# Kernel optimization log

Hardware: AMD Instinct MI355X
Metric: run time of the kernel (lower is better)

## Reference

```python
import jax, jax.numpy as jnp
import numpy as np

B, S, D = 4, 2048, 1024
H, Dh = 16, 64


def setup_inputs() -> dict:
    key = jax.random.key(0)
    ks = jax.random.split(key, 9)
    s_in = 1.0 / np.sqrt(D)
    inp = {
        "key": jax.random.normal(ks[0], (B, S, D), jnp.float32),
        "value": jax.random.normal(ks[1], (B, S, D), jnp.float32),
        "query": jax.random.normal(ks[2], (B, S, D), jnp.float32),
        # Linear weights stored as [in, out] (math-equivalent to torch W.T)
        "Wq": jax.random.uniform(ks[3], (D, H * Dh), jnp.float32, -s_in, s_in),
        "bq": jax.random.uniform(ks[4], (H * Dh,), jnp.float32, -s_in, s_in),
        "Wk": jax.random.uniform(ks[5], (D, H * Dh), jnp.float32, -s_in, s_in),
        "bk": jax.random.uniform(ks[6], (H * Dh,), jnp.float32, -s_in, s_in),
        "Wv": jax.random.uniform(ks[7], (D, H * Dh), jnp.float32, -s_in, s_in),
        "bv": jax.random.uniform(ks[8], (H * Dh,), jnp.float32, -s_in, s_in),
    }
    return inp


def reference(key, value, query, Wq, bq, Wk, bk, Wv, bv):
    b, s, _ = key.shape
    # projections -> [B, H, S, Dh]
    q = (query @ Wq + bq).reshape(b, s, H, Dh).transpose(0, 2, 1, 3)
    k = (key @ Wk + bk).reshape(b, s, H, Dh).transpose(0, 2, 1, 3)
    v = (value @ Wv + bv).reshape(b, s, H, Dh).transpose(0, 2, 1, 3)
    scores = jnp.einsum("bhqd,bhkd->bhqk", q, k) / np.sqrt(Dh).astype(np.float32)
    p = jax.nn.softmax(scores, axis=-1)
    out = jnp.einsum("bhqk,bhkd->bhqd", p, v)  # [B, H, S, Dh]
    return out.transpose(0, 2, 1, 3).reshape(b, s, H * Dh)
```

## Files before the change

kernel.cpp:

```cpp
#include <hip/hip_runtime.h>

typedef __bf16 bf16;
typedef __bf16 bf16x8 __attribute__((ext_vector_type(8)));
typedef __bf16 bf16x4 __attribute__((ext_vector_type(4)));
typedef _Float16 f16x4 __attribute__((ext_vector_type(4)));
typedef float  f32x4  __attribute__((ext_vector_type(4)));

#define LOG2E 1.44269504088896340736f
#define SCQ (0.125f * LOG2E)

__device__ __forceinline__ void async16(const void* g, void* l) {
  __builtin_amdgcn_global_load_lds(
      (const __attribute__((address_space(1))) unsigned int*)g,
      (__attribute__((address_space(3))) unsigned int*)l, 16, 0, 0);
}

__device__ __forceinline__ f32x4 mfma_bf16(bf16x8 a, bf16x8 b, f32x4 c) {
  return __builtin_amdgcn_mfma_f32_16x16x32_bf16(a, b, c, 0, 0, 0);
}
__device__ __forceinline__ f32x4 mfma_f16k16(f16x4 a, f16x4 b, f32x4 c) {
  return __builtin_amdgcn_mfma_f32_16x16x16f16(a, b, c, 0, 0, 0);
}

__global__ __launch_bounds__(256) void cvt3(const float* __restrict__ q,
                                            const float* __restrict__ k,
                                            const float* __restrict__ v,
                                            bf16* __restrict__ out) {
  int z = blockIdx.y;
  const float* in = z == 0 ? q : (z == 1 ? k : v);
  bf16* o = out + (size_t)z * 8388608;
  int i = blockIdx.x * 256 + threadIdx.x;
  const float4* p = (const float4*)in;
  float4 a = p[i * 2], c = p[i * 2 + 1];
  bf16x8 r;
  r[0] = (bf16)a.x; r[1] = (bf16)a.y; r[2] = (bf16)a.z; r[3] = (bf16)a.w;
  r[4] = (bf16)c.x; r[5] = (bf16)c.y; r[6] = (bf16)c.z; r[7] = (bf16)c.w;
  ((bf16x8*)o)[i] = r;
}

__global__ __launch_bounds__(256) void wtrans(const float* __restrict__ W0,
                                              const float* __restrict__ W1,
                                              const float* __restrict__ W2,
                                              bf16* __restrict__ Wt) {
  const float* W = blockIdx.z == 0 ? W0 : (blockIdx.z == 1 ? W1 : W2);
  bf16* O = Wt + (size_t)blockIdx.z * (1024 * 1024);
  __shared__ float t[64 * 69];
  int tid = threadIdx.x;
  int k0 = blockIdx.x * 64, n0 = blockIdx.y * 64;
  int r0 = tid >> 4, c0 = (tid & 15) * 4;
#pragma unroll
  for (int rr = 0; rr < 4; rr++) {
    int k = r0 + rr * 16;
    float4 v = *(const float4*)(W + (k0 + k) * 1024 + n0 + c0);
    t[k * 69 + c0 + 0] = v.x; t[k * 69 + c0 + 1] = v.y;
    t[k * 69 + c0 + 2] = v.z; t[k * 69 + c0 + 3] = v.w;
  }
  __syncthreads();
#pragma unroll
  for (int rr = 0; rr < 4; rr++) {
    int n = r0 + rr * 16;
    bf16x4 o;
#pragma unroll
    for (int j = 0; j < 4; j++) o[j] = (bf16)t[(c0 + j) * 69 + n];
    *(bf16x4*)(O + (n0 + n) * 1024 + k0 + c0) = o;
  }
}

__global__ __launch_bounds__(256) void gemm_qkv(const bf16* __restrict__ Act,
                                                const bf16* __restrict__ Wt,
                                                const float* __restrict__ b0,
                                                const float* __restrict__ b1,
                                                const float* __restrict__ b2,
                                                bf16* __restrict__ qo,
                                                bf16* __restrict__ ko,
                                                _Float16* __restrict__ vf) {
  __shared__ bf16 smem[16384];
  bf16* sA = smem;
  bf16* sB = smem + 8192;
  const int tid = threadIdx.x;
  const int wave = tid >> 6, lane = tid & 63;
  const int quad = lane >> 4, l15 = lane & 15;
  const int z = blockIdx.z;
  const int m0 = blockIdx.x * 128, n0 = blockIdx.y * 128;
  const bf16* A = Act + (size_t)z * 8388608;
  const bf16* Bt = Wt + (size_t)z * 1048576;
  const float* bias = z == 0 ? b0 : (z == 1 ? b1 : b2);

  const bf16* ap[4]; const bf16* bp[4]; int lo[4];
#pragma unroll
  for (int i = 0; i < 4; i++) {
    int g = wave * 256 + i * 64 + lane;
    int row = g >> 3, jl = (g & 7) ^ (row & 7);
    ap[i] = A + (m0 + row) * 1024 + jl * 8;
    bp[i] = Bt + (n0 + row) * 1024 + jl * 8;
    lo[i] = (wave * 256 + i * 64) * 8;
  }
  const int wm = (wave & 1) * 64, wn = (wave >> 1) * 64;
  f32x4 acc[4][4] = {};

  for (int kt = 0; kt < 16; kt++) {
    const int ko_ = kt * 64;
#pragma unroll
    for (int i = 0; i < 4; i++) async16(ap[i] + ko_, sA + lo[i]);
#pragma unroll
    for (int i = 0; i < 4; i++) async16(bp[i] + ko_, sB + lo[i]);
    __syncthreads();
#pragma unroll
    for (int ks = 0; ks < 2; ks++) {
      bf16x8 af[4], bv[4];
#pragma unroll
      for (int mt = 0; mt < 4; mt++) {
        int m = wm + mt * 16 + l15;
        int ph = (ks * 4 + quad) ^ (m & 7);
        af[mt] = *(const bf16x8*)(sA + m * 64 + ph * 8);
      }
#pragma unroll
      for (int nt = 0; nt < 4; nt++) {
        int n = wn + nt * 16 + l15;
        int ph = (ks * 4 + quad) ^ (n & 7);
        bv[nt] = *(const bf16x8*)(sB + n * 64 + ph * 8);
      }
#pragma unroll
      for (int mt = 0; mt < 4; mt++)
#pragma unroll
        for (int nt = 0; nt < 4; nt++)
          acc[mt][nt] = mfma_bf16(af[mt], bv[nt], acc[mt][nt]);
    }
    __syncthreads();
  }

  if (z != 2) {
    bf16* O = z == 0 ? qo : ko;
    const float sc = z == 0 ? SCQ : 1.0f;
#pragma unroll
    for (int nt = 0; nt < 4; nt++) {
      int n = n0 + wn + nt * 16 + l15;
      float bc = bias[n];
#pragma unroll
      for (int mt = 0; mt < 4; mt++)
#pragma unroll
        for (int r = 0; r < 4; r++) {
          int m = m0 + wm + mt * 16 + quad * 4 + r;
          O[m * 1024 + n] = (bf16)((acc[mt][nt][r] + bc) * sc);
        }
    }
  } else {
    const int b = m0 >> 11, s0 = m0 & 2047;
    const int kvb = (s0 + wm) >> 6;
#pragma unroll
    for (int nt = 0; nt < 4; nt++) {
      int nn = n0 + wn + nt * 16;
      int h = nn >> 6, dt = (nn >> 4) & 3;
      float bc = bias[nn + l15];
#pragma unroll
      for (int mt = 0; mt < 4; mt++) {
        f16x4 pk;
#pragma unroll
        for (int r = 0; r < 4; r++) pk[r] = (_Float16)(acc[mt][nt][r] + bc);
        size_t off = ((((size_t)(b * 16 + h) * 32 + kvb) * 16 + (mt * 4 + dt)) * 64 + lane) * 4;
        *(f16x4*)(vf + off) = pk;
      }
    }
  }
}

__global__ __launch_bounds__(256) void attn(const bf16* __restrict__ Q,
                                            const bf16* __restrict__ K,
                                            const _Float16* __restrict__ VF,
                                            float* __restrict__ Out) {
  __shared__ bf16 sQ[8192];
  __shared__ bf16 sK[2][4096];
  __shared__ _Float16 sV[2][4096];
  const int tid = threadIdx.x;
  const int wave = tid >> 6, lane = tid & 63;
  const int quad = lane >> 4, l15 = lane & 15;
  const int q0 = blockIdx.x * 128, h = blockIdx.y, b = blockIdx.z;
  const bf16* Kbase = K + (size_t)(b * 2048) * 1024 + h * 64;
  const _Float16* Vbase = VF + (size_t)(b * 16 + h) * 131072;

#pragma unroll
  for (int i = 0; i < 4; i++) {
    int g = i * 256 + tid;
    int row = g >> 3, jl = (g & 7) ^ (row & 7);
    async16(Q + (size_t)(b * 2048 + q0 + row) * 1024 + h * 64 + jl * 8, sQ + g * 8);
  }
#pragma unroll
  for (int i = 0; i < 2; i++) {
    int g = i * 256 + tid;
    int row = g >> 3, jl = (g & 7) ^ (row & 7);
    async16(Kbase + row * 1024 + jl * 8, sK[0] + g * 8);
    async16(Vbase + g * 8, sV[0] + g * 8);
  }
  __syncthreads();

  bf16x8 qf[2][2];
#pragma unroll
  for (int qt2 = 0; qt2 < 2; qt2++)
#pragma unroll
    for (int ks = 0; ks < 2; ks++) {
      int m = wave * 32 + qt2 * 16 + l15;
      int ph = (ks * 4 + quad) ^ (l15 & 7);
      qf[qt2][ks] = *(const bf16x8*)(sQ + m * 64 + ph * 8);
    }

  f32x4 oaccT[2][4] = {};
  float ls[2] = {0.f, 0.f};

  const int ph0 = quad ^ (l15 & 7), ph1 = (4 + quad) ^ (l15 & 7);

  for (int kvb = 0; kvb < 32; kvb++) {
    const int cur = kvb & 1;
    if (kvb < 31) {
      int kn = (kvb + 1) * 64;
#pragma unroll
      for (int i = 0; i < 2; i++) {
        int g = i * 256 + tid;
        int row = g >> 3, jl = (g & 7) ^ (row & 7);
        async16(Kbase + (size_t)(kn + row) * 1024 + jl * 8, sK[cur ^ 1] + g * 8);
        async16(Vbase + (kvb + 1) * 4096 + g * 8, sV[cur ^ 1] + g * 8);
      }
    }
    const bf16* sKc = sK[cur];
    const _Float16* sVc = sV[cur];
#pragma unroll
    for (int t = 0; t < 4; t++) {
      int row = t * 16 + l15;
      bf16x8 kf0 = *(const bf16x8*)(sKc + row * 64 + ph0 * 8);
      bf16x8 kf1 = *(const bf16x8*)(sKc + row * 64 + ph1 * 8);
      f32x4 st0 = {}, st1 = {};
      st0 = mfma_bf16(kf0, qf[0][0], st0);
      st0 = mfma_bf16(kf1, qf[0][1], st0);
      st1 = mfma_bf16(kf0, qf[1][0], st1);
      st1 = mfma_bf16(kf1, qf[1][1], st1);
      f16x4 pf0, pf1;
#pragma unroll
      for (int r = 0; r < 4; r++) {
        float p0 = __builtin_amdgcn_exp2f(st0[r]);
        float p1 = __builtin_amdgcn_exp2f(st1[r]);
        ls[0] += p0; ls[1] += p1;
        pf0[r] = (_Float16)p0; pf1[r] = (_Float16)p1;
      }
#pragma unroll
      for (int dt = 0; dt < 4; dt++) {
        f16x4 va = *(const f16x4*)(sVc + ((t * 4 + dt) * 64 + lane) * 4);
        oaccT[0][dt] = mfma_f16k16(va, pf0, oaccT[0][dt]);
        oaccT[1][dt] = mfma_f16k16(va, pf1, oaccT[1][dt]);
      }
    }
    __syncthreads();
  }

#pragma unroll
  for (int qt2 = 0; qt2 < 2; qt2++) {
    float l = ls[qt2];
    l += __shfl_xor(l, 16);
    l += __shfl_xor(l, 32);
    float inv = 1.f / l;
    int qrow = b * 2048 + q0 + wave * 32 + qt2 * 16 + l15;
#pragma unroll
    for (int dt = 0; dt < 4; dt++) {
      float4 v;
      v.x = oaccT[qt2][dt][0] * inv;
      v.y = oaccT[qt2][dt][1] * inv;
      v.z = oaccT[qt2][dt][2] * inv;
      v.w = oaccT[qt2][dt][3] * inv;
      *(float4*)(Out + (size_t)qrow * 1024 + h * 64 + dt * 16 + quad * 4) = v;
    }
  }
}

extern "C" void kernel_launch(void* const* d_in, const int* in_sizes, int n_in,
                              void* d_out, int out_size, void* d_ws, size_t ws_size,
                              hipStream_t stream) {
  const float* key   = (const float*)d_in[0];
  const float* value = (const float*)d_in[1];
  const float* query = (const float*)d_in[2];
  const float* Wq = (const float*)d_in[3];
  const float* bq = (const float*)d_in[4];
  const float* Wk = (const float*)d_in[5];
  const float* bk = (const float*)d_in[6];
  const float* Wv = (const float*)d_in[7];
  const float* bv = (const float*)d_in[8];
  float* out = (float*)d_out;

  char* ws = (char*)d_ws;
  bf16* actb   = (bf16*)(ws);
  bf16* wt     = (bf16*)(ws + 50331648);
  bf16* qo     = (bf16*)(ws + 56623104);
  bf16* ko     = (bf16*)(ws + 73400320);
  _Float16* vf = (_Float16*)(ws + 90177536);
  (void)in_sizes; (void)n_in; (void)out_size; (void)ws_size;

  wtrans<<<dim3(16, 16, 3), 256, 0, stream>>>(Wq, Wk, Wv, wt);
  cvt3<<<dim3(4096, 3), 256, 0, stream>>>(query, key, value, actb);
  gemm_qkv<<<dim3(64, 8, 3), 256, 0, stream>>>(actb, wt, bq, bk, bv, qo, ko, vf);
  attn<<<dim3(16, 16, 4), 256, 0, stream>>>(qo, ko, vf, out);
}
```

Measured before the change: 335.6 us.

## Enlarge GEMM tile to 128x256 with swizzled grid; single-buffer 128-key attention tiles

The QKV GEMM now computes 128x256 tiles per block, with each wave holding a 64x128 accumulator. Block indices are remapped through a swizzle for L2 locality, the launch gets min-blocks hints, and the grid is halved. The attention kernel drops K/V double-buffering in favour of single 128-key tiles loaded synchronously after each tile is consumed, with an occupancy hint of 4 blocks. This cuts per-tile overhead and barrier count, but loses load/compute overlap within a block and raises register pressure.

```diff
diff --git a/kernel.cpp b/kernel.cpp
--- a/kernel.cpp
+++ b/kernel.cpp
@@ -66,48 +66,58 @@
   }
 }
 
-__global__ __launch_bounds__(256) void gemm_qkv(const bf16* __restrict__ Act,
-                                                const bf16* __restrict__ Wt,
-                                                const float* __restrict__ b0,
-                                                const float* __restrict__ b1,
-                                                const float* __restrict__ b2,
-                                                bf16* __restrict__ qo,
-                                                bf16* __restrict__ ko,
-                                                _Float16* __restrict__ vf) {
-  __shared__ bf16 smem[16384];
+__global__ __launch_bounds__(256, 2) void gemm_qkv(const bf16* __restrict__ Act,
+                                                   const bf16* __restrict__ Wt,
+                                                   const float* __restrict__ b0,
+                                                   const float* __restrict__ b1,
+                                                   const float* __restrict__ b2,
+                                                   bf16* __restrict__ qo,
+                                                   bf16* __restrict__ ko,
+                                                   _Float16* __restrict__ vf) {
+  __shared__ bf16 smem[24576];
   bf16* sA = smem;
   bf16* sB = smem + 8192;
   const int tid = threadIdx.x;
   const int wave = tid >> 6, lane = tid & 63;
   const int quad = lane >> 4, l15 = lane & 15;
   const int z = blockIdx.z;
-  const int m0 = blockIdx.x * 128, n0 = blockIdx.y * 128;
+  const int lin = blockIdx.y * 64 + blockIdx.x;
+  const int tx = (lin & 7) | ((lin >> 5) << 3);
+  const int ty = (lin >> 3) & 3;
+  const int m0 = tx * 128, n0 = ty * 256;
   const bf16* A = Act + (size_t)z * 8388608;
   const bf16* Bt = Wt + (size_t)z * 1048576;
   const float* bias = z == 0 ? b0 : (z == 1 ? b1 : b2);
 
-  const bf16* ap[4]; const bf16* bp[4]; int lo[4];
+  const bf16* ap[4]; int loa[4];
+  const bf16* bp[8]; int lob[8];
 #pragma unroll
   for (int i = 0; i < 4; i++) {
     int g = wave * 256 + i * 64 + lane;
     int row = g >> 3, jl = (g & 7) ^ (row & 7);
     ap[i] = A + (m0 + row) * 1024 + jl * 8;
+    loa[i] = (wave * 256 + i * 64) * 8;
+  }
+#pragma unroll
+  for (int i = 0; i < 8; i++) {
+    int g = wave * 512 + i * 64 + lane;
+    int row = g >> 3, jl = (g & 7) ^ (row & 7);
     bp[i] = Bt + (n0 + row) * 1024 + jl * 8;
-    lo[i] = (wave * 256 + i * 64) * 8;
-  }
-  const int wm = (wave & 1) * 64, wn = (wave >> 1) * 64;
-  f32x4 acc[4][4] = {};
+    lob[i] = (wave * 512 + i * 64) * 8;
+  }
+  const int wm = (wave & 1) * 64, wn = (wave >> 1) * 128;
+  f32x4 acc[4][8] = {};
 
   for (int kt = 0; kt < 16; kt++) {
     const int ko_ = kt * 64;
 #pragma unroll
-    for (int i = 0; i < 4; i++) async16(ap[i] + ko_, sA + lo[i]);
-#pragma unroll
-    for (int i = 0; i < 4; i++) async16(bp[i] + ko_, sB + lo[i]);
+    for (int i = 0; i < 4; i++) async16(ap[i] + ko_, sA + loa[i]);
+#pragma unroll
+    for (int i = 0; i < 8; i++) async16(bp[i] + ko_, sB + lob[i]);
     __syncthreads();
 #pragma unroll
     for (int ks = 0; ks < 2; ks++) {
-      bf16x8 af[4], bv[4];
+      bf16x8 af[4];
 #pragma unroll
       for (int mt = 0; mt < 4; mt++) {
         int m = wm + mt * 16 + l15;
@@ -115,16 +125,20 @@
         af[mt] = *(const bf16x8*)(sA + m * 64 + ph * 8);
       }
 #pragma unroll
-      for (int nt = 0; nt < 4; nt++) {
-        int n = wn + nt * 16 + l15;
-        int ph = (ks * 4 + quad) ^ (n & 7);
-        bv[nt] = *(const bf16x8*)(sB + n * 64 + ph * 8);
-      }
-#pragma unroll
-      for (int mt = 0; mt < 4; mt++)
-#pragma unroll
-        for (int nt = 0; nt < 4; nt++)
-          acc[mt][nt] = mfma_bf16(af[mt], bv[nt], acc[mt][nt]);
+      for (int nh = 0; nh < 2; nh++) {
+        bf16x8 bv[4];
+#pragma unroll
+        for (int nt = 0; nt < 4; nt++) {
+          int n = wn + (nh * 4 + nt) * 16 + l15;
+          int ph = (ks * 4 + quad) ^ (n & 7);
+          bv[nt] = *(const bf16x8*)(sB + n * 64 + ph * 8);
+        }
+#pragma unroll
+        for (int mt = 0; mt < 4; mt++)
+#pragma unroll
+          for (int nt = 0; nt < 4; nt++)
+            acc[mt][nh * 4 + nt] = mfma_bf16(af[mt], bv[nt], acc[mt][nh * 4 + nt]);
+      }
     }
     __syncthreads();
   }
@@ -133,7 +147,7 @@
     bf16* O = z == 0 ? qo : ko;
     const float sc = z == 0 ? SCQ : 1.0f;
 #pragma unroll
-    for (int nt = 0; nt < 4; nt++) {
+    for (int nt = 0; nt < 8; nt++) {
       int n = n0 + wn + nt * 16 + l15;
       float bc = bias[n];
 #pragma unroll
@@ -148,7 +162,7 @@
     const int b = m0 >> 11, s0 = m0 & 2047;
     const int kvb = (s0 + wm) >> 6;
 #pragma unroll
-    for (int nt = 0; nt < 4; nt++) {
+    for (int nt = 0; nt < 8; nt++) {
       int nn = n0 + wn + nt * 16;
       int h = nn >> 6, dt = (nn >> 4) & 3;
       float bc = bias[nn + l15];
@@ -164,13 +178,13 @@
   }
 }
 
-__global__ __launch_bounds__(256) void attn(const bf16* __restrict__ Q,
-                                            const bf16* __restrict__ K,
-                                            const _Float16* __restrict__ VF,
-                                            float* __restrict__ Out) {
+__global__ __launch_bounds__(256, 4) void attn(const bf16* __restrict__ Q,
+                                               const bf16* __restrict__ K,
+                                               const _Float16* __restrict__ VF,
+                                               float* __restrict__ Out) {
   __shared__ bf16 sQ[8192];
-  __shared__ bf16 sK[2][4096];
-  __shared__ _Float16 sV[2][4096];
+  __shared__ bf16 sK[8192];
+  __shared__ _Float16 sV[8192];
   const int tid = threadIdx.x;
   const int wave = tid >> 6, lane = tid & 63;
   const int quad = lane >> 4, l15 = lane & 15;
@@ -183,13 +197,8 @@
     int g = i * 256 + tid;
     int row = g >> 3, jl = (g & 7) ^ (row & 7);
     async16(Q + (size_t)(b * 2048 + q0 + row) * 1024 + h * 64 + jl * 8, sQ + g * 8);
-  }
-#pragma unroll
-  for (int i = 0; i < 2; i++) {
-    int g = i * 256 + tid;
-    int row = g >> 3, jl = (g & 7) ^ (row & 7);
-    async16(Kbase + row * 1024 + jl * 8, sK[0] + g * 8);
-    async16(Vbase + g * 8, sV[0] + g * 8);
+    async16(Kbase + (size_t)row * 1024 + jl * 8, sK + g * 8);
+    async16(Vbase + g * 8, sV + g * 8);
   }
   __syncthreads();
 
@@ -205,28 +214,14 @@
 
   f32x4 oaccT[2][4] = {};
   float ls[2] = {0.f, 0.f};
-
   const int ph0 = quad ^ (l15 & 7), ph1 = (4 + quad) ^ (l15 & 7);
 
-  for (int kvb = 0; kvb < 32; kvb++) {
-    const int cur = kvb & 1;
-    if (kvb < 31) {
-      int kn = (kvb + 1) * 64;
-#pragma unroll
-      for (int i = 0; i < 2; i++) {
-        int g = i * 256 + tid;
-        int row = g >> 3, jl = (g & 7) ^ (row & 7);
-        async16(Kbase + (size_t)(kn + row) * 1024 + jl * 8, sK[cur ^ 1] + g * 8);
-        async16(Vbase + (kvb + 1) * 4096 + g * 8, sV[cur ^ 1] + g * 8);
-      }
-    }
-    const bf16* sKc = sK[cur];
-    const _Float16* sVc = sV[cur];
-#pragma unroll
-    for (int t = 0; t < 4; t++) {
+  for (int kvb = 0; kvb < 16; kvb++) {
+#pragma unroll
+    for (int t = 0; t < 8; t++) {
       int row = t * 16 + l15;
-      bf16x8 kf0 = *(const bf16x8*)(sKc + row * 64 + ph0 * 8);
-      bf16x8 kf1 = *(const bf16x8*)(sKc + row * 64 + ph1 * 8);
+      bf16x8 kf0 = *(const bf16x8*)(sK + row * 64 + ph0 * 8);
+      bf16x8 kf1 = *(const bf16x8*)(sK + row * 64 + ph1 * 8);
       f32x4 st0 = {}, st1 = {};
       st0 = mfma_bf16(kf0, qf[0][0], st0);
       st0 = mfma_bf16(kf1, qf[0][1], st0);
@@ -240,14 +235,27 @@
         ls[0] += p0; ls[1] += p1;
         pf0[r] = (_Float16)p0; pf1[r] = (_Float16)p1;
       }
+      const _Float16* sVt = sV + (t >> 2) * 4096;
+      int tl = (t & 3) * 4;
 #pragma unroll
       for (int dt = 0; dt < 4; dt++) {
-        f16x4 va = *(const f16x4*)(sVc + ((t * 4 + dt) * 64 + lane) * 4);
+        f16x4 va = *(const f16x4*)(sVt + ((tl + dt) * 64 + lane) * 4);
         oaccT[0][dt] = mfma_f16k16(va, pf0, oaccT[0][dt]);
         oaccT[1][dt] = mfma_f16k16(va, pf1, oaccT[1][dt]);
       }
     }
     __syncthreads();
+    if (kvb < 15) {
+      int kn = (kvb + 1) * 128;
+#pragma unroll
+      for (int i = 0; i < 4; i++) {
+        int g = i * 256 + tid;
+        int row = g >> 3, jl = (g & 7) ^ (row & 7);
+        async16(Kbase + (size_t)(kn + row) * 1024 + jl * 8, sK + g * 8);
+        async16(Vbase + (kvb + 1) * 8192 + g * 8, sV + g * 8);
+      }
+      __syncthreads();
+    }
   }
 
 #pragma unroll
@@ -293,6 +301,6 @@
 
   wtrans<<<dim3(16, 16, 3), 256, 0, stream>>>(Wq, Wk, Wv, wt);
   cvt3<<<dim3(4096, 3), 256, 0, stream>>>(query, key, value, actb);
-  gemm_qkv<<<dim3(64, 8, 3), 256, 0, stream>>>(actb, wt, bq, bk, bv, qo, ko, vf);
+  gemm_qkv<<<dim3(64, 4, 3), 256, 0, stream>>>(actb, wt, bq, bk, bv, qo, ko, vf);
   attn<<<dim3(16, 16, 4), 256, 0, stream>>>(qo, ko, vf, out);
 }
```

Result: faster. 314.0 us (-6.4%).

## Merge prep kernels, widen V layout, single-buffer 128-row KV tiles in attention

Applied to the files above, without the earlier changes.

The weight-transpose and activation-convert kernels are merged into one launch to save a kernel launch. The V projection output is repacked into 8-wide f16 fragments so attention loads V with 16-byte reads. Attention switches from a double-buffered 64-row KV pipeline to a single-buffered 128-row tile with a sync before and after each refill, halving the number of iterations. Occupancy hints are added to both GEMM and attention launch bounds. The cost is that KV loads no longer overlap with compute, so attention relies on multiple resident blocks per CU to hide that latency.

```diff
diff --git a/kernel.cpp b/kernel.cpp
--- a/kernel.cpp
+++ b/kernel.cpp
@@ -4,6 +4,7 @@
 typedef __bf16 bf16x8 __attribute__((ext_vector_type(8)));
 typedef __bf16 bf16x4 __attribute__((ext_vector_type(4)));
 typedef _Float16 f16x4 __attribute__((ext_vector_type(4)));
+typedef _Float16 f16x8 __attribute__((ext_vector_type(8)));
 typedef float  f32x4  __attribute__((ext_vector_type(4)));
 
 #define LOG2E 1.44269504088896340736f
@@ -22,58 +23,59 @@
   return __builtin_amdgcn_mfma_f32_16x16x16f16(a, b, c, 0, 0, 0);
 }
 
-__global__ __launch_bounds__(256) void cvt3(const float* __restrict__ q,
+__global__ __launch_bounds__(256) void prep(const float* __restrict__ q,
                                             const float* __restrict__ k,
                                             const float* __restrict__ v,
-                                            bf16* __restrict__ out) {
-  int z = blockIdx.y;
-  const float* in = z == 0 ? q : (z == 1 ? k : v);
-  bf16* o = out + (size_t)z * 8388608;
-  int i = blockIdx.x * 256 + threadIdx.x;
-  const float4* p = (const float4*)in;
-  float4 a = p[i * 2], c = p[i * 2 + 1];
-  bf16x8 r;
-  r[0] = (bf16)a.x; r[1] = (bf16)a.y; r[2] = (bf16)a.z; r[3] = (bf16)a.w;
-  r[4] = (bf16)c.x; r[5] = (bf16)c.y; r[6] = (bf16)c.z; r[7] = (bf16)c.w;
-  ((bf16x8*)o)[i] = r;
-}
-
-__global__ __launch_bounds__(256) void wtrans(const float* __restrict__ W0,
-                                              const float* __restrict__ W1,
-                                              const float* __restrict__ W2,
-                                              bf16* __restrict__ Wt) {
-  const float* W = blockIdx.z == 0 ? W0 : (blockIdx.z == 1 ? W1 : W2);
-  bf16* O = Wt + (size_t)blockIdx.z * (1024 * 1024);
+                                            const float* __restrict__ W0,
+                                            const float* __restrict__ W1,
+                                            const float* __restrict__ W2,
+                                            bf16* __restrict__ actb,
+                                            bf16* __restrict__ Wt) {
   __shared__ float t[64 * 69];
-  int tid = threadIdx.x;
-  int k0 = blockIdx.x * 64, n0 = blockIdx.y * 64;
-  int r0 = tid >> 4, c0 = (tid & 15) * 4;
-#pragma unroll
-  for (int rr = 0; rr < 4; rr++) {
-    int k = r0 + rr * 16;
-    float4 v = *(const float4*)(W + (k0 + k) * 1024 + n0 + c0);
-    t[k * 69 + c0 + 0] = v.x; t[k * 69 + c0 + 1] = v.y;
-    t[k * 69 + c0 + 2] = v.z; t[k * 69 + c0 + 3] = v.w;
-  }
-  __syncthreads();
-#pragma unroll
-  for (int rr = 0; rr < 4; rr++) {
-    int n = r0 + rr * 16;
-    bf16x4 o;
-#pragma unroll
-    for (int j = 0; j < 4; j++) o[j] = (bf16)t[(c0 + j) * 69 + n];
-    *(bf16x4*)(O + (n0 + n) * 1024 + k0 + c0) = o;
-  }
-}
-
-__global__ __launch_bounds__(256) void gemm_qkv(const bf16* __restrict__ Act,
-                                                const bf16* __restrict__ Wt,
-                                                const float* __restrict__ b0,
-                                                const float* __restrict__ b1,
-                                                const float* __restrict__ b2,
-                                                bf16* __restrict__ qo,
-                                                bf16* __restrict__ ko,
-                                                _Float16* __restrict__ vf) {
+  const int z = blockIdx.y, tid = threadIdx.x;
+  if (blockIdx.x < 4096) {
+    const float* in = z == 0 ? q : (z == 1 ? k : v);
+    bf16* o = actb + (size_t)z * 8388608;
+    int i = blockIdx.x * 256 + tid;
+    const float4* p = (const float4*)in;
+    float4 a = p[i * 2], c = p[i * 2 + 1];
+    bf16x8 r;
+    r[0] = (bf16)a.x; r[1] = (bf16)a.y; r[2] = (bf16)a.z; r[3] = (bf16)a.w;
+    r[4] = (bf16)c.x; r[5] = (bf16)c.y; r[6] = (bf16)c.z; r[7] = (bf16)c.w;
+    ((bf16x8*)o)[i] = r;
+  } else {
+    const float* W = z == 0 ? W0 : (z == 1 ? W1 : W2);
+    bf16* O = Wt + (size_t)z * (1024 * 1024);
+    int lin = blockIdx.x - 4096;
+    int k0 = (lin & 15) * 64, n0 = (lin >> 4) * 64;
+    int r0 = tid >> 4, c0 = (tid & 15) * 4;
+#pragma unroll
+    for (int rr = 0; rr < 4; rr++) {
+      int kk = r0 + rr * 16;
+      float4 vv = *(const float4*)(W + (k0 + kk) * 1024 + n0 + c0);
+      t[kk * 69 + c0 + 0] = vv.x; t[kk * 69 + c0 + 1] = vv.y;
+      t[kk * 69 + c0 + 2] = vv.z; t[kk * 69 + c0 + 3] = vv.w;
+    }
+    __syncthreads();
+#pragma unroll
+    for (int rr = 0; rr < 4; rr++) {
+      int n = r0 + rr * 16;
+      bf16x4 o;
+#pragma unroll
+      for (int j = 0; j < 4; j++) o[j] = (bf16)t[(c0 + j) * 69 + n];
+      *(bf16x4*)(O + (n0 + n) * 1024 + k0 + c0) = o;
+    }
+  }
+}
+
+__global__ __launch_bounds__(256, 3) void gemm_qkv(const bf16* __restrict__ Act,
+                                                   const bf16* __restrict__ Wt,
+                                                   const float* __restrict__ b0,
+                                                   const float* __restrict__ b1,
+                                                   const float* __restrict__ b2,
+                                                   bf16* __restrict__ qo,
+                                                   bf16* __restrict__ ko,
+                                                   _Float16* __restrict__ vf) {
   __shared__ bf16 smem[16384];
   bf16* sA = smem;
   bf16* sB = smem + 8192;
@@ -146,31 +148,35 @@
     }
   } else {
     const int b = m0 >> 11, s0 = m0 & 2047;
-    const int kvb = (s0 + wm) >> 6;
-#pragma unroll
-    for (int nt = 0; nt < 4; nt++) {
-      int nn = n0 + wn + nt * 16;
-      int h = nn >> 6, dt = (nn >> 4) & 3;
-      float bc = bias[nn + l15];
+    const int kvb64 = (s0 + wm) >> 6;
+#pragma unroll
+    for (int k2 = 0; k2 < 2; k2++) {
+      int nn = n0 + wn + k2 * 32;
+      int h = nn >> 6, np = (nn >> 5) & 1;
+      float bc0 = bias[nn + l15];
+      float bc1 = bias[nn + 16 + l15];
 #pragma unroll
       for (int mt = 0; mt < 4; mt++) {
-        f16x4 pk;
-#pragma unroll
-        for (int r = 0; r < 4; r++) pk[r] = (_Float16)(acc[mt][nt][r] + bc);
-        size_t off = ((((size_t)(b * 16 + h) * 32 + kvb) * 16 + (mt * 4 + dt)) * 64 + lane) * 4;
-        *(f16x4*)(vf + off) = pk;
-      }
-    }
-  }
-}
-
-__global__ __launch_bounds__(256) void attn(const bf16* __restrict__ Q,
-                                            const bf16* __restrict__ K,
-                                            const _Float16* __restrict__ VF,
-                                            float* __restrict__ Out) {
+        f16x8 pk;
+#pragma unroll
+        for (int r = 0; r < 4; r++) {
+          pk[r]     = (_Float16)(acc[mt][2 * k2][r] + bc0);
+          pk[4 + r] = (_Float16)(acc[mt][2 * k2 + 1][r] + bc1);
+        }
+        size_t off = ((((size_t)(b * 16 + h) * 32 + kvb64) * 8 + (mt * 2 + np)) * 64 + lane) * 8;
+        *(f16x8*)(vf + off) = pk;
+      }
+    }
+  }
+}
+
+__global__ __launch_bounds__(256, 4) void attn(const bf16* __restrict__ Q,
+                                               const bf16* __restrict__ K,
+                                               const _Float16* __restrict__ VF,
+                                               float* __restrict__ Out) {
   __shared__ bf16 sQ[8192];
-  __shared__ bf16 sK[2][4096];
-  __shared__ _Float16 sV[2][4096];
+  __shared__ bf16 sK[8192];
+  __shared__ _Float16 sV[8192];
   const int tid = threadIdx.x;
   const int wave = tid >> 6, lane = tid & 63;
   const int quad = lane >> 4, l15 = lane & 15;
@@ -183,13 +189,8 @@
     int g = i * 256 + tid;
     int row = g >> 3, jl = (g & 7) ^ (row & 7);
     async16(Q + (size_t)(b * 2048 + q0 + row) * 1024 + h * 64 + jl * 8, sQ + g * 8);
-  }
-#pragma unroll
-  for (int i = 0; i < 2; i++) {
-    int g = i * 256 + tid;
-    int row = g >> 3, jl = (g & 7) ^ (row & 7);
-    async16(Kbase + row * 1024 + jl * 8, sK[0] + g * 8);
-    async16(Vbase + g * 8, sV[0] + g * 8);
+    async16(Kbase + (size_t)row * 1024 + jl * 8, sK + g * 8);
+    async16(Vbase + g * 8, sV + g * 8);
   }
   __syncthreads();
 
@@ -205,28 +206,14 @@
 
   f32x4 oaccT[2][4] = {};
   float ls[2] = {0.f, 0.f};
-
   const int ph0 = quad ^ (l15 & 7), ph1 = (4 + quad) ^ (l15 & 7);
 
-  for (int kvb = 0; kvb < 32; kvb++) {
-    const int cur = kvb & 1;
-    if (kvb < 31) {
-      int kn = (kvb + 1) * 64;
-#pragma unroll
-      for (int i = 0; i < 2; i++) {
-        int g = i * 256 + tid;
-        int row = g >> 3, jl = (g & 7) ^ (row & 7);
-        async16(Kbase + (size_t)(kn + row) * 1024 + jl * 8, sK[cur ^ 1] + g * 8);
-        async16(Vbase + (kvb + 1) * 4096 + g * 8, sV[cur ^ 1] + g * 8);
-      }
-    }
-    const bf16* sKc = sK[cur];
-    const _Float16* sVc = sV[cur];
-#pragma unroll
-    for (int t = 0; t < 4; t++) {
+  for (int kvb = 0; kvb < 16; kvb++) {
+#pragma unroll
+    for (int t = 0; t < 8; t++) {
       int row = t * 16 + l15;
-      bf16x8 kf0 = *(const bf16x8*)(sKc + row * 64 + ph0 * 8);
-      bf16x8 kf1 = *(const bf16x8*)(sKc + row * 64 + ph1 * 8);
+      bf16x8 kf0 = *(const bf16x8*)(sK + row * 64 + ph0 * 8);
+      bf16x8 kf1 = *(const bf16x8*)(sK + row * 64 + ph1 * 8);
       f32x4 st0 = {}, st1 = {};
       st0 = mfma_bf16(kf0, qf[0][0], st0);
       st0 = mfma_bf16(kf1, qf[0][1], st0);
@@ -240,14 +227,30 @@
         ls[0] += p0; ls[1] += p1;
         pf0[r] = (_Float16)p0; pf1[r] = (_Float16)p1;
       }
-#pragma unroll
-      for (int dt = 0; dt < 4; dt++) {
-        f16x4 va = *(const f16x4*)(sVc + ((t * 4 + dt) * 64 + lane) * 4);
-        oaccT[0][dt] = mfma_f16k16(va, pf0, oaccT[0][dt]);
-        oaccT[1][dt] = mfma_f16k16(va, pf1, oaccT[1][dt]);
+      const _Float16* sVt = sV + (t >> 2) * 4096 + (t & 3) * 1024;
+#pragma unroll
+      for (int np = 0; np < 2; np++) {
+        f16x8 va2 = *(const f16x8*)(sVt + np * 512 + lane * 8);
+        f16x4 lo = __builtin_shufflevector(va2, va2, 0, 1, 2, 3);
+        f16x4 hi = __builtin_shufflevector(va2, va2, 4, 5, 6, 7);
+        oaccT[0][2 * np]     = mfma_f16k16(lo, pf0, oaccT[0][2 * np]);
+        oaccT[0][2 * np + 1] = mfma_f16k16(hi, pf0, oaccT[0][2 * np + 1]);
+        oaccT[1][2 * np]     = mfma_f16k16(lo, pf1, oaccT[1][2 * np]);
+        oaccT[1][2 * np + 1] = mfma_f16k16(hi, pf1, oaccT[1][2 * np + 1]);
       }
     }
     __syncthreads();
+    if (kvb < 15) {
+      int kn = (kvb + 1) * 128;
+#pragma unroll
+      for (int i = 0; i < 4; i++) {
+        int g = i * 256 + tid;
+        int row = g >> 3, jl = (g & 7) ^ (row & 7);
+        async16(Kbase + (size_t)(kn + row) * 1024 + jl * 8, sK + g * 8);
+        async16(Vbase + (kvb + 1) * 8192 + g * 8, sV + g * 8);
+      }
+      __syncthreads();
+    }
   }
 
 #pragma unroll
@@ -291,8 +294,7 @@
   _Float16* vf = (_Float16*)(ws + 90177536);
   (void)in_sizes; (void)n_in; (void)out_size; (void)ws_size;
 
-  wtrans<<<dim3(16, 16, 3), 256, 0, stream>>>(Wq, Wk, Wv, wt);
-  cvt3<<<dim3(4096, 3), 256, 0, stream>>>(query, key, value, actb);
+  prep<<<dim3(4352, 3), 256, 0, stream>>>(query, key, value, Wq, Wk, Wv, actb, wt);
   gemm_qkv<<<dim3(64, 8, 3), 256, 0, stream>>>(actb, wt, bq, bk, bv, qo, ko, vf);
   attn<<<dim3(16, 16, 4), 256, 0, stream>>>(qo, ko, vf, out);
 }
```

Result: faster. 304.7 us (-9.2%).
